# Performance work log

Hardware: AMD Instinct MI355X
Metric: run time of the kernel (lower is better)

## Reference

```python
import jax, jax.numpy as jnp
import numpy as np

B, S, F, D, VOCAB, H = 1024, 512, 4, 32, 100001, 64
LN_EPS = 1e-3  # keras LayerNormalization default


def setup_inputs() -> dict:
    key = jax.random.key(0)
    ks = jax.random.split(key, 16)
    sd = 0.05
    return {
        "values": jax.random.normal(ks[0], (B, S, F), jnp.float32),
        "names": jax.random.randint(ks[1], (B, S), 0, VOCAB),
        "emb_table": jax.random.normal(ks[2], (VOCAB, D), jnp.float32) * sd,
        "W_num": jax.random.normal(ks[3], (F, D), jnp.float32) * sd,
        "b_num": jnp.zeros((D,), jnp.float32),
        "Wq": jax.random.normal(ks[4], (D, D), jnp.float32) * sd,
        "bq": jnp.zeros((D,), jnp.float32),
        "Wv": jax.random.normal(ks[5], (D, D), jnp.float32) * sd,
        "bv": jnp.zeros((D,), jnp.float32),
        "attn_scale": jnp.ones((D,), jnp.float32),
        "Wp": jax.random.normal(ks[6], (D, H), jnp.float32) * sd,
        "bp": jnp.zeros((H,), jnp.float32),
        "ln_gamma": jnp.ones((H,), jnp.float32),
        "ln_beta": jnp.zeros((H,), jnp.float32),
        "Ws": jax.random.normal(ks[7], (H, 2), jnp.float32) * sd,
    }


def reference(values, names, emb_table, W_num, b_num, Wq, bq, Wv, bv,
              attn_scale, Wp, bp, ln_gamma, ln_beta, Ws):
    # embeddings + numerical projection  [B,S,D]
    v = values @ W_num + b_num
    e = emb_table[names]
    mix = e + v
    # query from last position, value/key from the rest
    q = mix[:, -1:, :] @ Wq + bq          # [B,1,D]
    val = mix[:, :-1, :] @ Wv + bv        # [B,S-1,D]
    # keras AdditiveAttention (use_scale=True): score = sum(scale*tanh(q+k))
    scores = jnp.sum(attn_scale * jnp.tanh(q[:, :, None, :] + val[:, None, :, :]), axis=-1)  # [B,1,S-1]
    attn = jax.nn.softmax(scores, axis=-1)
    emb_out = jnp.einsum('bij,bjd->bid', attn, val)  # [B,1,D]
    # broadcast add then mean over sequence
    context = jnp.mean(emb_out + mix, axis=1)        # [B,D]
    # predictor: Dense(relu) + LayerNorm(axis=1 == features)
    h = jax.nn.relu(context @ Wp + bp)               # [B,H]
    mu = jnp.mean(h, axis=1, keepdims=True)
    var = jnp.var(h, axis=1, keepdims=True)
    h = (h - mu) * jax.lax.rsqrt(var + LN_EPS) * ln_gamma + ln_beta
    # scorer: Dense(2, softmax, no bias)
    score = jax.nn.softmax(h @ Ws, axis=-1)          # [B,2]
    return (score, emb_out, attn, h)
```

## Files before the change

kernel.cpp:

```cpp
#include <hip/hip_runtime.h>
#include <hip/hip_bf16.h>
#include <math.h>

constexpr int Bsz   = 1024;
constexpr int S     = 512;
constexpr int SV    = 511;
constexpr int D     = 32;
constexpr int F     = 4;
constexpr int H     = 64;
constexpr int BDIM  = 256;
constexpr int VOCAB = 100001;
constexpr size_t TAB_BYTES = (size_t)VOCAB * 64 * 2;

__device__ __forceinline__ float fast_tanh(float x) {
  const float ex = __expf(2.f * x);
  return 1.f - 2.f * __builtin_amdgcn_rcpf(ex + 1.f);
}

__device__ __forceinline__ void unpack4(uint2 u, float* f) {
  f[0] = __uint_as_float(u.x << 16); f[1] = __uint_as_float(u.x & 0xffff0000u);
  f[2] = __uint_as_float(u.y << 16); f[3] = __uint_as_float(u.y & 0xffff0000u);
}

__device__ __forceinline__ void unpack8(uint4 u, float* f) {
  f[0] = __uint_as_float(u.x << 16); f[1] = __uint_as_float(u.x & 0xffff0000u);
  f[2] = __uint_as_float(u.y << 16); f[3] = __uint_as_float(u.y & 0xffff0000u);
  f[4] = __uint_as_float(u.z << 16); f[5] = __uint_as_float(u.z & 0xffff0000u);
  f[6] = __uint_as_float(u.w << 16); f[7] = __uint_as_float(u.w & 0xffff0000u);
}

__global__ __launch_bounds__(BDIM) void build_tab(
    const float* __restrict__ emb, const float* __restrict__ Wv,
    const float* __restrict__ W_num, const float* __restrict__ b_num,
    const float* __restrict__ bv,
    __hip_bfloat16* __restrict__ T, float* __restrict__ wsc)
{
  __shared__ float sWv[D * D];
  for (int i = threadIdx.x; i < D * D; i += BDIM) sWv[i] = Wv[i];
  __syncthreads();

  if (blockIdx.x == gridDim.x - 1) {
    const int tid = threadIdx.x;
    if (tid < F * D) {
      const int f = tid >> 5, k = tid & 31;
      float a = 0.f;
      #pragma unroll
      for (int m = 0; m < D; m++) a += W_num[f * D + m] * sWv[m * D + k];
      wsc[k * 4 + f] = a;
    } else if (tid < F * D + D) {
      const int k = tid - F * D;
      float a = bv[k];
      #pragma unroll
      for (int m = 0; m < D; m++) a += b_num[m] * sWv[m * D + k];
      wsc[F * D + k] = a;
    }
    return;
  }

  const int lr = threadIdx.x >> 5, k = threadIdx.x & 31;
  const int row = blockIdx.x * 8 + lr;
  if (row < VOCAB) {
    const float4* e4 = reinterpret_cast<const float4*>(emb + (size_t)row * D);
    float a = 0.f;
    #pragma unroll
    for (int c = 0; c < 8; c++) {
      const float4 v = e4[c];
      a += v.x * sWv[(4 * c + 0) * D + k] + v.y * sWv[(4 * c + 1) * D + k]
         + v.z * sWv[(4 * c + 2) * D + k] + v.w * sWv[(4 * c + 3) * D + k];
    }
    T[(size_t)row * 64 + k]      = __float2bfloat16(emb[(size_t)row * D + k]);
    T[(size_t)row * 64 + 32 + k] = __float2bfloat16(a);
  }
}

__global__ __launch_bounds__(BDIM) void attn_main(
    const float* __restrict__ values, const int* __restrict__ names,
    const __hip_bfloat16* __restrict__ T, const float* __restrict__ wsc,
    const float* __restrict__ emb,
    const float* __restrict__ W_num, const float* __restrict__ b_num,
    const float* __restrict__ Wq,    const float* __restrict__ bq,
    const float* __restrict__ attn_scale,
    const float* __restrict__ Wp,    const float* __restrict__ bp,
    const float* __restrict__ ln_g,  const float* __restrict__ ln_b,
    const float* __restrict__ Ws,
    float* __restrict__ out_score, float* __restrict__ out_emb,
    float* __restrict__ out_attn,  float* __restrict__ out_h)
{
  __shared__ float sW2T[D][4];
  __shared__ float sQS[D][2];
  __shared__ float smixq[D];
  __shared__ float sred[4][69];
  __shared__ float sctx[D];
  __shared__ float sL[1];
  __shared__ float sE[512];
  __shared__ int   sNames[512];

  const int b = blockIdx.x, tid = threadIdx.x, lane = tid & 63, wv = tid >> 6;
  const int kl = lane & 7, rg = lane >> 3;
  const int rbase = wv * 8 + rg;

  reinterpret_cast<int2*>(sNames)[tid] = *reinterpret_cast<const int2*>(names + (size_t)b * S + tid * 2);
  if (tid < 128) sW2T[tid >> 2][tid & 3] = wsc[tid];
  if (tid < D) {
    const int    nq = names[(size_t)b * S + (S - 1)];
    const float* vr = values + (size_t)(b * S + (S - 1)) * F;
    smixq[tid] = emb[(size_t)nq * D + tid] + b_num[tid]
               + vr[0] * W_num[tid] + vr[1] * W_num[D + tid]
               + vr[2] * W_num[2 * D + tid] + vr[3] * W_num[3 * D + tid];
  }
  __syncthreads();
  if (tid < D) {
    float a = bq[tid];
    #pragma unroll
    for (int m = 0; m < D; m++) a += smixq[m] * Wq[m * D + tid];
    sQS[tid][0] = a + wsc[128 + tid];
    sQS[tid][1] = attn_scale[tid];
  }
  __syncthreads();

  float qb[4], scl[4], w2a[4], w2b[4], w2c[4], w2d[4];
  #pragma unroll
  for (int i = 0; i < 4; i++) {
    const int k = kl * 4 + i;
    qb[i]  = sQS[k][0]; scl[i] = sQS[k][1];
    w2a[i] = sW2T[k][0]; w2b[i] = sW2T[k][1];
    w2c[i] = sW2T[k][2]; w2d[i] = sW2T[k][3];
  }

  float esum[4] = {0.f, 0.f, 0.f, 0.f}, acc[4] = {0.f, 0.f, 0.f, 0.f};
  float lloc = 0.f, vs0 = 0.f, vs1 = 0.f, vs2 = 0.f, vs3 = 0.f;

  const char* Tb = (const char*)T;
  uint2 Eb[4], Wb[4]; float4 vb[4];

  #define ISSUE(P, ST) do {                                                    \
    const int   j_  = (P) * 32 + rbase;                                        \
    const int   nm_ = sNames[j_];                                              \
    const char* pr_ = Tb + (size_t)nm_ * 128 + kl * 8;                         \
    Eb[ST] = *(const uint2*)pr_;                                               \
    Wb[ST] = *(const uint2*)(pr_ + 64);                                        \
    vb[ST] = *reinterpret_cast<const float4*>(values + (size_t)(b * S + j_) * F); \
  } while (0)

  ISSUE(0, 0); ISSUE(1, 1); ISSUE(2, 2);

  #pragma unroll
  for (int p = 0; p < 16; p++) {
    const int st = p & 3;
    float em[4], w[4], t[4];
    unpack4(Eb[st], em); unpack4(Wb[st], w);
    const float4 vv = vb[st];
    if (p + 3 < 16) { const int sn = (p + 3) & 3; ISSUE(p + 3, sn); }
    float s = 0.f;
    #pragma unroll
    for (int i = 0; i < 4; i++) {
      t[i] = w[i] + qb[i] + vv.x * w2a[i] + vv.y * w2b[i]
           + vv.z * w2c[i] + vv.w * w2d[i];
      s += scl[i] * fast_tanh(t[i]);
    }
    s += __shfl_xor(s, 1); s += __shfl_xor(s, 2); s += __shfl_xor(s, 4);
    const bool  valid = (p * 32 + rbase) < SV;
    const float e = valid ? __expf(s) : 0.f;
    lloc += e;
    if (kl == 0) sE[p * 32 + rbase] = e;
    if (valid) {
      vs0 += vv.x; vs1 += vv.y; vs2 += vv.z; vs3 += vv.w;
      #pragma unroll
      for (int i = 0; i < 4; i++) esum[i] += em[i];
    }
    #pragma unroll
    for (int i = 0; i < 4; i++) acc[i] = fmaf(e, t[i], acc[i]);
  }
  #undef ISSUE

  #pragma unroll
  for (int off = 8; off < 64; off <<= 1) {
    lloc += __shfl_xor(lloc, off);
    vs0 += __shfl_xor(vs0, off); vs1 += __shfl_xor(vs1, off);
    vs2 += __shfl_xor(vs2, off); vs3 += __shfl_xor(vs3, off);
    #pragma unroll
    for (int i = 0; i < 4; i++) {
      acc[i]  += __shfl_xor(acc[i], off);
      esum[i] += __shfl_xor(esum[i], off);
    }
  }
  if (lane < 8) {
    #pragma unroll
    for (int i = 0; i < 4; i++) {
      sred[wv][lane * 4 + i]      = acc[i];
      sred[wv][32 + lane * 4 + i] = esum[i];
    }
  }
  if (lane == 0) {
    sred[wv][64] = lloc;
    sred[wv][65] = vs0; sred[wv][66] = vs1; sred[wv][67] = vs2; sred[wv][68] = vs3;
  }
  __syncthreads();
  if (tid == 0) sL[0] = sred[0][64] + sred[1][64] + sred[2][64] + sred[3][64];
  __syncthreads();
  const float invL = 1.f / sL[0];

  for (int idx = tid; idx < SV; idx += BDIM)
    out_attn[(size_t)b * SV + idx] = sE[idx] * invL;

  if (tid < D) {
    const float aS = sred[0][tid] + sred[1][tid] + sred[2][tid] + sred[3][tid];
    const float eS = sred[0][D + tid] + sred[1][D + tid] + sred[2][D + tid] + sred[3][D + tid];
    float vp = 0.f;
    #pragma unroll
    for (int f = 0; f < 4; f++) {
      const float vf = sred[0][65 + f] + sred[1][65 + f] + sred[2][65 + f] + sred[3][65 + f];
      vp += vf * W_num[f * D + tid];
    }
    const float q  = sQS[tid][0] - wsc[128 + tid];
    const float eo = aS * invL - q;
    out_emb[(size_t)b * D + tid] = eo;
    sctx[tid] = eo + (eS + vp + (float)SV * b_num[tid] + smixq[tid]) * (1.f / (float)S);
  }
  __syncthreads();

  if (tid < H) {
    float hv = bp[tid];
    #pragma unroll
    for (int d = 0; d < D; d++) hv += sctx[d] * Wp[d * H + tid];
    hv = fmaxf(hv, 0.f);
    float mu = hv;
    #pragma unroll
    for (int off = 32; off; off >>= 1) mu += __shfl_xor(mu, off);
    mu *= (1.f / 64.f);
    const float dv = hv - mu;
    float vvv = dv * dv;
    #pragma unroll
    for (int off = 32; off; off >>= 1) vvv += __shfl_xor(vvv, off);
    vvv *= (1.f / 64.f);
    const float hn = dv * rsqrtf(vvv + 1e-3f) * ln_g[tid] + ln_b[tid];
    out_h[(size_t)b * H + tid] = hn;
    float s0 = hn * Ws[2 * tid], s1 = hn * Ws[2 * tid + 1];
    #pragma unroll
    for (int off = 32; off; off >>= 1) { s0 += __shfl_xor(s0, off); s1 += __shfl_xor(s1, off); }
    if (tid == 0) {
      const float mx = fmaxf(s0, s1);
      const float a0 = __expf(s0 - mx), a1 = __expf(s1 - mx);
      const float inv = 1.f / (a0 + a1);
      out_score[(size_t)b * 2]     = a0 * inv;
      out_score[(size_t)b * 2 + 1] = a1 * inv;
    }
  }
}

__global__ __launch_bounds__(BDIM) void attn_fused_gemv(
    const float* __restrict__ values, const int* __restrict__ names,
    const float* __restrict__ emb,
    const float* __restrict__ W_num, const float* __restrict__ b_num,
    const float* __restrict__ Wq,    const float* __restrict__ bq,
    const float* __restrict__ Wv,    const float* __restrict__ bv,
    const float* __restrict__ attn_scale,
    const float* __restrict__ Wp,    const float* __restrict__ bp,
    const float* __restrict__ ln_g,  const float* __restrict__ ln_b,
    const float* __restrict__ Ws,
    float* __restrict__ out_score, float* __restrict__ out_emb,
    float* __restrict__ out_attn,  float* __restrict__ out_h)
{
  __shared__ float sWnum[F * D];
  __shared__ float sbnum[D];
  __shared__ float sWq[D * D];
  __shared__ float sWv[D * D];
  __shared__ float sbv[D];
  __shared__ float sscale[D];
  __shared__ float sq[D];
  __shared__ float smixq[D];
  __shared__ float sred[4][2 * D];
  __shared__ float sredS[4];
  __shared__ float sML[2];
  __shared__ float sctx[D];
  __shared__ float sWp[D * H];

  const int b = blockIdx.x, tid = threadIdx.x, lane = tid & 63, wv = tid >> 6;

  for (int i = tid; i < F * D; i += BDIM) sWnum[i] = W_num[i];
  if (tid < D) { sbnum[tid] = b_num[tid]; sbv[tid] = bv[tid]; sscale[tid] = attn_scale[tid]; }
  for (int i = tid; i < D * D; i += BDIM) { sWq[i] = Wq[i]; sWv[i] = Wv[i]; }
  for (int i = tid; i < D * H; i += BDIM) sWp[i] = Wp[i];
  __syncthreads();

  if (tid < D) {
    const int    name = names[b * S + (S - 1)];
    const float* vr   = values + (size_t)(b * S + (S - 1)) * F;
    smixq[tid] = emb[(size_t)name * D + tid] + sbnum[tid]
               + vr[0] * sWnum[tid] + vr[1] * sWnum[D + tid]
               + vr[2] * sWnum[2 * D + tid] + vr[3] * sWnum[3 * D + tid];
  }
  __syncthreads();
  if (tid < D) {
    float a = bq[tid];
    #pragma unroll
    for (int k = 0; k < D; k++) a += smixq[k] * sWq[k * D + tid];
    sq[tid] = a;
  }
  __syncthreads();

  float msum[D], acc[D];
  #pragma unroll
  for (int k = 0; k < D; k++) { msum[k] = 0.f; acc[k] = 0.f; }
  float mloc = -INFINITY, lloc = 0.f;
  float sc0 = 0.f, sc1 = 0.f;
  const bool has2 = (tid < SV - BDIM);

  auto row = [&](int j, float& sout) {
    const int    name = names[b * S + j];
    const float4 v4   = *reinterpret_cast<const float4*>(values + (size_t)(b * S + j) * F);
    const float4* e4p = reinterpret_cast<const float4*>(emb + (size_t)name * D);
    float mix[D];
    #pragma unroll
    for (int c = 0; c < 8; c++) {
      const float4 e = e4p[c];
      mix[4 * c] = e.x; mix[4 * c + 1] = e.y; mix[4 * c + 2] = e.z; mix[4 * c + 3] = e.w;
    }
    #pragma unroll
    for (int k = 0; k < D; k++) {
      mix[k] += sbnum[k] + v4.x * sWnum[k] + v4.y * sWnum[D + k]
              + v4.z * sWnum[2 * D + k] + v4.w * sWnum[3 * D + k];
      msum[k] += mix[k];
    }
    float val[D];
    #pragma unroll
    for (int k = 0; k < D; k++) val[k] = sbv[k];
    for (int m = 0; m < D; m++) {
      const float mv = mix[m];
      #pragma unroll
      for (int k = 0; k < D; k++) val[k] += mv * sWv[m * D + k];
    }
    float s = 0.f;
    #pragma unroll
    for (int k = 0; k < D; k++) s += sscale[k] * fast_tanh(sq[k] + val[k]);
    sout = s;
    float w;
    if (s > mloc) {
      const float sf = __expf(mloc - s);
      lloc *= sf;
      #pragma unroll
      for (int k = 0; k < D; k++) acc[k] *= sf;
      mloc = s; w = 1.f;
    } else {
      w = __expf(s - mloc);
    }
    lloc += w;
    #pragma unroll
    for (int k = 0; k < D; k++) acc[k] += w * val[k];
  };

  row(tid, sc0);
  if (has2) row(tid + BDIM, sc1);

  float mw = mloc;
  #pragma unroll
  for (int off = 32; off; off >>= 1) mw = fmaxf(mw, __shfl_xor(mw, off));
  if (lane == 0) sredS[wv] = mw;
  __syncthreads();
  if (tid == 0) sML[0] = fmaxf(fmaxf(sredS[0], sredS[1]), fmaxf(sredS[2], sredS[3]));
  __syncthreads();
  const float M = sML[0];
  {
    const float adj = __expf(mloc - M);
    lloc *= adj;
    #pragma unroll
    for (int k = 0; k < D; k++) acc[k] *= adj;
  }
  float lw = lloc;
  #pragma unroll
  for (int off = 32; off; off >>= 1) lw += __shfl_xor(lw, off);
  if (lane == 0) sredS[wv] = lw;
  #pragma unroll
  for (int k = 0; k < D; k++) {
    float a = acc[k], mm = msum[k];
    #pragma unroll
    for (int off = 32; off; off >>= 1) { a += __shfl_xor(a, off); mm += __shfl_xor(mm, off); }
    if (lane == 0) { sred[wv][k] = a; sred[wv][D + k] = mm; }
  }
  __syncthreads();
  if (tid == 0) sML[1] = sredS[0] + sredS[1] + sredS[2] + sredS[3];
  __syncthreads();
  const float L = sML[1], invL = 1.f / L;

  out_attn[(size_t)b * SV + tid] = __expf(sc0 - M) * invL;
  if (has2) out_attn[(size_t)b * SV + tid + BDIM] = __expf(sc1 - M) * invL;

  if (tid < D) {
    const float a  = sred[0][tid] + sred[1][tid] + sred[2][tid] + sred[3][tid];
    const float mm = sred[0][D + tid] + sred[1][D + tid] + sred[2][D + tid] + sred[3][D + tid];
    const float eo = a * invL;
    out_emb[(size_t)b * D + tid] = eo;
    sctx[tid] = eo + (mm + smixq[tid]) * (1.f / (float)S);
  }
  __syncthreads();

  if (tid < H) {
    float hv = bp[tid];
    #pragma unroll
    for (int d = 0; d < D; d++) hv += sctx[d] * sWp[d * H + tid];
    hv = fmaxf(hv, 0.f);
    float mu = hv;
    #pragma unroll
    for (int off = 32; off; off >>= 1) mu += __shfl_xor(mu, off);
    mu *= (1.f / 64.f);
    const float dv = hv - mu;
    float vv = dv * dv;
    #pragma unroll
    for (int off = 32; off; off >>= 1) vv += __shfl_xor(vv, off);
    vv *= (1.f / 64.f);
    const float hn = dv * rsqrtf(vv + 1e-3f) * ln_g[tid] + ln_b[tid];
    out_h[(size_t)b * H + tid] = hn;
    float s0 = hn * Ws[2 * tid], s1 = hn * Ws[2 * tid + 1];
    #pragma unroll
    for (int off = 32; off; off >>= 1) { s0 += __shfl_xor(s0, off); s1 += __shfl_xor(s1, off); }
    if (tid == 0) {
      const float mx = fmaxf(s0, s1);
      const float a0 = __expf(s0 - mx), a1 = __expf(s1 - mx);
      const float inv = 1.f / (a0 + a1);
      out_score[(size_t)b * 2]     = a0 * inv;
      out_score[(size_t)b * 2 + 1] = a1 * inv;
    }
  }
}

extern "C" void kernel_launch(void* const* d_in, const int* in_sizes, int n_in,
                              void* d_out, int out_size, void* d_ws, size_t ws_size,
                              hipStream_t stream) {
  const float* values = (const float*)d_in[0];
  const int*   names  = (const int*)d_in[1];
  const float* emb    = (const float*)d_in[2];
  const float* W_num  = (const float*)d_in[3];
  const float* b_num  = (const float*)d_in[4];
  const float* Wq     = (const float*)d_in[5];
  const float* bq     = (const float*)d_in[6];
  const float* Wv     = (const float*)d_in[7];
  const float* bv     = (const float*)d_in[8];
  const float* scal   = (const float*)d_in[9];
  const float* Wp     = (const float*)d_in[10];
  const float* bp     = (const float*)d_in[11];
  const float* ln_g   = (const float*)d_in[12];
  const float* ln_b   = (const float*)d_in[13];
  const float* Ws     = (const float*)d_in[14];

  float* out      = (float*)d_out;
  float* o_score  = out;
  float* o_emb    = o_score + (size_t)Bsz * 2;
  float* o_attn   = o_emb   + (size_t)Bsz * D;
  float* o_h      = o_attn  + (size_t)Bsz * SV;

  const size_t need = TAB_BYTES + 256 * sizeof(float);
  if (ws_size >= need) {
    __hip_bfloat16* T = (__hip_bfloat16*)d_ws;
    float* wsc = (float*)((char*)d_ws + TAB_BYTES);
    hipLaunchKernelGGL(build_tab, dim3((VOCAB + 7) / 8 + 1), dim3(BDIM), 0, stream,
                       emb, Wv, W_num, b_num, bv, T, wsc);
    hipLaunchKernelGGL(attn_main, dim3(Bsz), dim3(BDIM), 0, stream,
                       values, names, T, wsc, emb, W_num, b_num, Wq, bq, scal,
                       Wp, bp, ln_g, ln_b, Ws, o_score, o_emb, o_attn, o_h);
  } else {
    hipLaunchKernelGGL(attn_fused_gemv, dim3(Bsz), dim3(BDIM), 0, stream,
                       values, names, emb, W_num, b_num, Wq, bq, Wv, bv, scal,
                       Wp, bp, ln_g, ln_b, Ws, o_score, o_emb, o_attn, o_h);
  }
}
```

Before: 132.6 us.

## Interleave bf16 table rows, stage values in LDS, deepen gather prefetch

```diff
diff --git a/kernel.cpp b/kernel.cpp
--- a/kernel.cpp
+++ b/kernel.cpp
@@ -17,16 +17,9 @@
   return 1.f - 2.f * __builtin_amdgcn_rcpf(ex + 1.f);
 }
 
-__device__ __forceinline__ void unpack4(uint2 u, float* f) {
-  f[0] = __uint_as_float(u.x << 16); f[1] = __uint_as_float(u.x & 0xffff0000u);
-  f[2] = __uint_as_float(u.y << 16); f[3] = __uint_as_float(u.y & 0xffff0000u);
-}
-
-__device__ __forceinline__ void unpack8(uint4 u, float* f) {
-  f[0] = __uint_as_float(u.x << 16); f[1] = __uint_as_float(u.x & 0xffff0000u);
-  f[2] = __uint_as_float(u.y << 16); f[3] = __uint_as_float(u.y & 0xffff0000u);
-  f[4] = __uint_as_float(u.z << 16); f[5] = __uint_as_float(u.z & 0xffff0000u);
-  f[6] = __uint_as_float(u.w << 16); f[7] = __uint_as_float(u.w & 0xffff0000u);
+__device__ __forceinline__ void unpack4(uint a, uint b, float* f) {
+  f[0] = __uint_as_float(a << 16); f[1] = __uint_as_float(a & 0xffff0000u);
+  f[2] = __uint_as_float(b << 16); f[3] = __uint_as_float(b & 0xffff0000u);
 }
 
 __global__ __launch_bounds__(BDIM) void build_tab(
@@ -68,8 +61,9 @@
       a += v.x * sWv[(4 * c + 0) * D + k] + v.y * sWv[(4 * c + 1) * D + k]
          + v.z * sWv[(4 * c + 2) * D + k] + v.w * sWv[(4 * c + 3) * D + k];
     }
-    T[(size_t)row * 64 + k]      = __float2bfloat16(emb[(size_t)row * D + k]);
-    T[(size_t)row * 64 + 32 + k] = __float2bfloat16(a);
+    const int blk = k >> 2, i = k & 3;
+    T[(size_t)row * 64 + blk * 8 + i]     = __float2bfloat16(emb[(size_t)row * D + k]);
+    T[(size_t)row * 64 + blk * 8 + 4 + i] = __float2bfloat16(a);
   }
 }
 
@@ -86,20 +80,26 @@
     float* __restrict__ out_score, float* __restrict__ out_emb,
     float* __restrict__ out_attn,  float* __restrict__ out_h)
 {
-  __shared__ float sW2T[D][4];
-  __shared__ float sQS[D][2];
-  __shared__ float smixq[D];
-  __shared__ float sred[4][69];
-  __shared__ float sctx[D];
-  __shared__ float sL[1];
-  __shared__ float sE[512];
-  __shared__ int   sNames[512];
+  __shared__ float  sW2T[D][4];
+  __shared__ float  sQS[D][2];
+  __shared__ float  smixq[D];
+  __shared__ float  sred[4][69];
+  __shared__ float  sctx[D];
+  __shared__ float  sL[1];
+  __shared__ float  sE[512];
+  __shared__ int    sNames[512];
+  __shared__ float4 sVals[512];
 
   const int b = blockIdx.x, tid = threadIdx.x, lane = tid & 63, wv = tid >> 6;
   const int kl = lane & 7, rg = lane >> 3;
   const int rbase = wv * 8 + rg;
 
   reinterpret_cast<int2*>(sNames)[tid] = *reinterpret_cast<const int2*>(names + (size_t)b * S + tid * 2);
+  {
+    const float4* v4p = reinterpret_cast<const float4*>(values + (size_t)b * S * F);
+    sVals[tid]       = v4p[tid];
+    sVals[tid + 256] = v4p[tid + 256];
+  }
   if (tid < 128) sW2T[tid >> 2][tid & 3] = wsc[tid];
   if (tid < D) {
     const int    nq = names[(size_t)b * S + (S - 1)];
@@ -131,26 +131,23 @@
   float lloc = 0.f, vs0 = 0.f, vs1 = 0.f, vs2 = 0.f, vs3 = 0.f;
 
   const char* Tb = (const char*)T;
-  uint2 Eb[4], Wb[4]; float4 vb[4];
-
-  #define ISSUE(P, ST) do {                                                    \
-    const int   j_  = (P) * 32 + rbase;                                        \
-    const int   nm_ = sNames[j_];                                              \
-    const char* pr_ = Tb + (size_t)nm_ * 128 + kl * 8;                         \
-    Eb[ST] = *(const uint2*)pr_;                                               \
-    Wb[ST] = *(const uint2*)(pr_ + 64);                                        \
-    vb[ST] = *reinterpret_cast<const float4*>(values + (size_t)(b * S + j_) * F); \
+  uint4 Gb[8];
+
+  #define ISSUE(P) do {                                                        \
+    const int nm_ = sNames[(P) * 32 + rbase];                                  \
+    Gb[(P) & 7] = *(const uint4*)(Tb + (size_t)nm_ * 128 + kl * 16);           \
   } while (0)
 
-  ISSUE(0, 0); ISSUE(1, 1); ISSUE(2, 2);
+  ISSUE(0); ISSUE(1); ISSUE(2); ISSUE(3); ISSUE(4); ISSUE(5); ISSUE(6);
 
   #pragma unroll
   for (int p = 0; p < 16; p++) {
-    const int st = p & 3;
+    const uint4 g = Gb[p & 7];
+    if (p + 7 < 16) ISSUE(p + 7);
     float em[4], w[4], t[4];
-    unpack4(Eb[st], em); unpack4(Wb[st], w);
-    const float4 vv = vb[st];
-    if (p + 3 < 16) { const int sn = (p + 3) & 3; ISSUE(p + 3, sn); }
+    unpack4(g.x, g.y, em);
+    unpack4(g.z, g.w, w);
+    const float4 vv = sVals[p * 32 + rbase];
     float s = 0.f;
     #pragma unroll
     for (int i = 0; i < 4; i++) {
```

New measurement: 134.1 us. About the same (+1.1%).
